# Kernel optimization log

Hardware: AMD Instinct MI355X
Metric: run time of the kernel (lower is better)

## Reference

```python
import jax, jax.numpy as jnp
import numpy as np

B, M, N, D = 32, 10, 1000, 128
DEMAND_SCALER, SPEED_SCALER, PREF_SCALER = 40.0, 1.0, 1.0


def _pos_encoding(m, d, dtype):
    # standard sinusoidal PE over agent positions 0..m-1
    pos = jnp.arange(m, dtype=dtype)[:, None]
    div = jnp.exp(jnp.arange(0, d, 2, dtype=dtype) * (-jnp.log(jnp.asarray(10000.0, dtype)) / d))
    ang = pos * div  # (m, d/2)
    return jnp.stack([jnp.sin(ang), jnp.cos(ang)], axis=-1).reshape(m, d)  # even=sin, odd=cos


def setup_inputs() -> dict:
    key = jax.random.key(0)
    ks = jax.random.split(key, 14)
    return {
        "locs": jax.random.uniform(ks[0], (B, M + N, 2), jnp.float32),
        "capacity": jax.random.uniform(ks[1], (B, M), jnp.float32),
        "speed": jax.random.uniform(ks[2], (B, M), jnp.float32),
        "demand": jax.random.uniform(ks[3], (B, 1, M + N), jnp.float32),
        "agents_preference": jax.random.uniform(ks[4], (B, M, M + N), jnp.float32),
        "action_mask": jnp.ones((B, M, M + N), dtype=bool),
        "W_depot": jax.random.normal(ks[5], (D, 2), jnp.float32) * 0.1,
        "W_posproj": jax.random.normal(ks[6], (D, D), jnp.float32) * 0.05,
        "alpha": jnp.ones((1,), jnp.float32),
        "W_agents": jax.random.normal(ks[7], (D, 4), jnp.float32) * 0.1,
        "W_depot_agents": jax.random.normal(ks[8], (D, 2 * D), jnp.float32) * 0.05,
        "W_clients": jax.random.normal(ks[9], (D, 5), jnp.float32) * 0.1,
        "W_pref": jax.random.normal(ks[10], (D, 1), jnp.float32) * 0.1,
        "W_final": jax.random.normal(ks[11], (D, 3 * D), jnp.float32) * 0.05,
    }


def reference(locs, capacity, speed, demand, agents_preference, action_mask,
              W_depot, W_posproj, alpha, W_agents, W_depot_agents, W_clients,
              W_pref, W_final):
    m = action_mask.shape[-2]
    d = W_final.shape[0]
    depot_locs = locs[:, :m]            # (B, m, 2)
    agents_locs = locs[:, :m]
    clients_locs = locs[:, m:]          # (B, N, 2)

    # depot branch with positional encoding
    dep_emb = depot_locs @ W_depot.T                                   # (B, m, D)
    pe = _pos_encoding(m, d, dep_emb.dtype)                            # (m, D)
    depot_embedding = dep_emb + alpha[0] * (pe @ W_posproj.T)          # broadcast over B

    # agents branch
    agents_feats = jnp.concatenate(
        [agents_locs, capacity[..., None] / DEMAND_SCALER, speed[..., None] / SPEED_SCALER], axis=-1)
    agents_embedding = agents_feats @ W_agents.T                       # (B, m, D)
    depot_agents_embedding = jnp.concatenate(
        [depot_embedding, agents_embedding], axis=-1) @ W_depot_agents.T  # (B, m, D)

    # clients branch (with polar feats)
    demands = demand[:, 0, m:]                                         # (B, N)
    centered = clients_locs - depot_locs[:, 0:1]                       # (B, N, 2)
    dist = jnp.linalg.norm(centered, axis=-1, keepdims=True)
    angle = jnp.arctan2(centered[..., 1:], centered[..., :1])
    clients_feats = jnp.concatenate(
        [clients_locs, demands[..., None] / DEMAND_SCALER, dist, angle], axis=-1)
    clients_embedding = clients_feats @ W_clients.T                    # (B, N, D)

    nodes_embedding = jnp.concatenate([agents_embedding, clients_embedding], axis=1)  # (B, m+N, D)

    # fused final projection: Linear(3D, D) on cat([nodes, pref_embed, depot_agents])
    # == nodes @ Wn.T  +  pref_embed @ Wp.T  +  depot_agents @ Wd.T, broadcast over dims.
    # pref_embed = pref[..., None] * W_pref[:, 0]  (rank-1), so pref_embed @ Wp.T = pref[..., None] * (Wp @ W_pref[:, 0])
    Wn, Wp, Wd = W_final[:, :d], W_final[:, d:2 * d], W_final[:, 2 * d:]
    v_pref = Wp @ W_pref[:, 0]                                         # (D,)
    pref = agents_preference / PREF_SCALER                             # (B, m, m+N)
    combined_embedding = (
        (nodes_embedding @ Wn.T)[:, None, :, :]                        # (B, 1, m+N, D)
        + pref[..., None] * v_pref                                     # (B, m, m+N, D)
        + (depot_agents_embedding @ Wd.T)[:, :, None, :]               # (B, m, 1, D)
    )
    return nodes_embedding, combined_embedding
```

## Files before the change

### kernel.cpp

```cpp
#include <hip/hip_runtime.h>
#include <math.h>

#define BB 32
#define MM 10
#define NNODES 1010
#define DD 128
#define RPB 32
#define NG 32

__global__ __launch_bounds__(256) void k_prep(
    const float* __restrict__ W_posproj,
    const float* __restrict__ W_da,
    const float* __restrict__ W_pref,
    const float* __restrict__ W_final,
    float* __restrict__ wnT,
    float* __restrict__ wdT,
    float* __restrict__ wdaT,
    float* __restrict__ vpref,
    float* __restrict__ peproj)
{
    const int bk = blockIdx.x;
    const int t = threadIdx.x;
    const int d = t & (DD - 1);
    const int h = t >> 7;

    if (bk < 16) {
        #pragma unroll
        for (int kk = 0; kk < 4; ++kk) {
            const int k = bk * 8 + h * 4 + kk;
            wnT[k * DD + d] = W_final[(size_t)d * 384 + k];
            wdT[k * DD + d] = W_final[(size_t)d * 384 + 256 + k];
        }
    } else if (bk < 32) {
        #pragma unroll
        for (int kk = 0; kk < 8; ++kk) {
            const int k = (bk - 16) * 16 + h * 8 + kk;
            wdaT[k * DD + d] = W_da[(size_t)d * 256 + k];
        }
    } else if (bk == 32) {
        if (t < DD) {
            float vp = 0.0f;
            const float4* w = (const float4*)(W_final + (size_t)d * 384 + DD);
            const float4* p = (const float4*)W_pref;
            #pragma unroll
            for (int k4 = 0; k4 < 32; ++k4) {
                const float4 a = w[k4], b = p[k4];
                vp = fmaf(a.x, b.x, fmaf(a.y, b.y, fmaf(a.z, b.z, fmaf(a.w, b.w, vp))));
            }
            vpref[d] = vp;
        }
    } else {
        const int m = bk - 33;
        __shared__ float pe_s[DD];
        if (t < DD) {
            const int i = d >> 1;
            const float div = expf((float)(2 * i) * (-logf(10000.0f) / (float)DD));
            const float ang = (float)m * div;
            pe_s[d] = (d & 1) ? cosf(ang) : sinf(ang);
        }
        __syncthreads();
        if (t < DD) {
            float pp = 0.0f;
            const float4* w = (const float4*)(W_posproj + (size_t)d * DD);
            const float4* p = (const float4*)pe_s;
            #pragma unroll
            for (int k4 = 0; k4 < 32; ++k4) {
                const float4 a = w[k4], b = p[k4];
                pp = fmaf(a.x, b.x, fmaf(a.y, b.y, fmaf(a.z, b.z, fmaf(a.w, b.w, pp))));
            }
            peproj[m * DD + d] = pp;
        }
    }
}

__global__ __launch_bounds__(256) void k_agents(
    const float* __restrict__ locs,
    const float* __restrict__ capacity,
    const float* __restrict__ speed,
    const float* __restrict__ W_depot,
    const float* __restrict__ alpha,
    const float* __restrict__ W_agents,
    const float* __restrict__ wdaT,
    const float* __restrict__ wdT,
    const float* __restrict__ peproj,
    float* __restrict__ out_nodes,
    float* __restrict__ ws_daWd)
{
    const int b = blockIdx.x / MM;
    const int m = blockIdx.x % MM;
    const int t = threadIdx.x;
    const int d = t & (DD - 1);
    const int h = t >> 7;

    __shared__ float cat_s[2 * DD];
    __shared__ float da_s[DD];
    __shared__ float part[2][DD];

    if (h == 0) {
        const float lx = locs[((size_t)b * NNODES + m) * 2 + 0];
        const float ly = locs[((size_t)b * NNODES + m) * 2 + 1];
        const float dep = fmaf(lx, W_depot[d * 2 + 0],
                          fmaf(ly, W_depot[d * 2 + 1],
                               alpha[0] * peproj[m * DD + d]));
        const float cap = capacity[b * MM + m] * (1.0f / 40.0f);
        const float spd = speed[b * MM + m];
        const float ag = fmaf(lx, W_agents[d * 4 + 0],
                         fmaf(ly, W_agents[d * 4 + 1],
                         fmaf(cap, W_agents[d * 4 + 2],
                              spd * W_agents[d * 4 + 3])));
        out_nodes[((size_t)b * NNODES + m) * DD + d] = ag;
        cat_s[d] = dep;
        cat_s[DD + d] = ag;
    }
    __syncthreads();

    {
        float a0 = 0.f, a1 = 0.f, a2 = 0.f, a3 = 0.f;
        const float* wp = wdaT + (size_t)(h * DD) * DD + d;
        const float* cp = cat_s + h * DD;
        #pragma unroll 8
        for (int k = 0; k < DD; k += 4) {
            a0 = fmaf(cp[k + 0], wp[(size_t)(k + 0) * DD], a0);
            a1 = fmaf(cp[k + 1], wp[(size_t)(k + 1) * DD], a1);
            a2 = fmaf(cp[k + 2], wp[(size_t)(k + 2) * DD], a2);
            a3 = fmaf(cp[k + 3], wp[(size_t)(k + 3) * DD], a3);
        }
        part[h][d] = (a0 + a1) + (a2 + a3);
    }
    __syncthreads();
    if (h == 0) da_s[d] = part[0][d] + part[1][d];
    __syncthreads();

    {
        float a0 = 0.f, a1 = 0.f, a2 = 0.f, a3 = 0.f;
        const float* wp = wdT + (size_t)(h * 64) * DD + d;
        const float* cp = da_s + h * 64;
        #pragma unroll 4
        for (int k = 0; k < 64; k += 4) {
            a0 = fmaf(cp[k + 0], wp[(size_t)(k + 0) * DD], a0);
            a1 = fmaf(cp[k + 1], wp[(size_t)(k + 1) * DD], a1);
            a2 = fmaf(cp[k + 2], wp[(size_t)(k + 2) * DD], a2);
            a3 = fmaf(cp[k + 3], wp[(size_t)(k + 3) * DD], a3);
        }
        part[h][d] = (a0 + a1) + (a2 + a3);
    }
    __syncthreads();
    if (h == 0)
        ws_daWd[(b * MM + m) * DD + d] = part[0][d] + part[1][d];
}

__global__ __launch_bounds__(256) void k_main(
    const float* __restrict__ locs,
    const float* __restrict__ demand,
    const float* __restrict__ pref,
    const float* __restrict__ W_clients,
    const float* __restrict__ wnT,
    const float* __restrict__ ws_daWd,
    const float* __restrict__ ws_vpref,
    float* __restrict__ out_nodes,
    float* __restrict__ out_comb)
{
    const int g = blockIdx.x;
    const int b = blockIdx.y;
    const int t = threadIdx.x;
    const int n0 = g * RPB;

    __shared__ float rows[RPB][DD];
    __shared__ float feat[RPB][5];
    __shared__ float pref_s[MM][RPB];

    if (t < RPB) {
        const int node = n0 + t;
        if (node < NNODES && node >= MM) {
            const float cx = locs[((size_t)b * NNODES + node) * 2 + 0];
            const float cy = locs[((size_t)b * NNODES + node) * 2 + 1];
            const float d0x = locs[((size_t)b * NNODES + 0) * 2 + 0];
            const float d0y = locs[((size_t)b * NNODES + 0) * 2 + 1];
            const float dx = cx - d0x;
            const float dy = cy - d0y;
            feat[t][0] = cx;
            feat[t][1] = cy;
            feat[t][2] = demand[(size_t)b * NNODES + node] * (1.0f / 40.0f);
            feat[t][3] = sqrtf(fmaf(dx, dx, dy * dy));
            feat[t][4] = atan2f(dy, dx);
        }
    }
    for (int idx = t; idx < MM * RPB; idx += 256) {
        const int mm = idx >> 5;
        const int rr = idx & 31;
        const int node = n0 + rr;
        pref_s[mm][rr] = (node < NNODES)
            ? pref[(size_t)(b * MM + mm) * NNODES + node] : 0.0f;
    }
    __syncthreads();

    {
        const int d = t & (DD - 1);
        const int h = t >> 7;
        const float wc0 = W_clients[d * 5 + 0];
        const float wc1 = W_clients[d * 5 + 1];
        const float wc2 = W_clients[d * 5 + 2];
        const float wc3 = W_clients[d * 5 + 3];
        const float wc4 = W_clients[d * 5 + 4];
        #pragma unroll
        for (int i = 0; i < RPB / 2; ++i) {
            const int r = h * (RPB / 2) + i;
            const int node = n0 + r;
            float val = 0.0f;
            if (node < NNODES) {
                if (node < MM) {
                    val = out_nodes[((size_t)b * NNODES + node) * DD + d];
                } else {
                    val = fmaf(feat[r][0], wc0,
                          fmaf(feat[r][1], wc1,
                          fmaf(feat[r][2], wc2,
                          fmaf(feat[r][3], wc3,
                               feat[r][4] * wc4))));
                    out_nodes[((size_t)b * NNODES + node) * DD + d] = val;
                }
            }
            rows[r][d] = val;
        }
    }
    __syncthreads();

    const int c = t & 31;
    const int s = t >> 5;
    const int col = c * 4;
    float4 acc[4];
    #pragma unroll
    for (int j = 0; j < 4; ++j) acc[j] = make_float4(0.f, 0.f, 0.f, 0.f);

    {
        const float* wt = wnT + col;
        #pragma unroll 2
        for (int k4 = 0; k4 < DD / 4; ++k4) {
            const float4 w0 = *(const float4*)(wt + (size_t)(k4 * 4 + 0) * DD);
            const float4 w1 = *(const float4*)(wt + (size_t)(k4 * 4 + 1) * DD);
            const float4 w2 = *(const float4*)(wt + (size_t)(k4 * 4 + 2) * DD);
            const float4 w3 = *(const float4*)(wt + (size_t)(k4 * 4 + 3) * DD);
            #pragma unroll
            for (int j = 0; j < 4; ++j) {
                const float4 x = *(const float4*)&rows[s * 4 + j][k4 * 4];
                acc[j].x = fmaf(x.x, w0.x, fmaf(x.y, w1.x,
                           fmaf(x.z, w2.x, fmaf(x.w, w3.x, acc[j].x))));
                acc[j].y = fmaf(x.x, w0.y, fmaf(x.y, w1.y,
                           fmaf(x.z, w2.y, fmaf(x.w, w3.y, acc[j].y))));
                acc[j].z = fmaf(x.x, w0.z, fmaf(x.y, w1.z,
                           fmaf(x.z, w2.z, fmaf(x.w, w3.z, acc[j].z))));
                acc[j].w = fmaf(x.x, w0.w, fmaf(x.y, w1.w,
                           fmaf(x.z, w2.w, fmaf(x.w, w3.w, acc[j].w))));
            }
        }
    }

    const float4 vp = *(const float4*)(ws_vpref + col);
    float4 dawd[MM];
    #pragma unroll
    for (int mm = 0; mm < MM; ++mm)
        dawd[mm] = *(const float4*)(ws_daWd + (size_t)(b * MM + mm) * DD + col);

    #pragma unroll
    for (int mm = 0; mm < MM; ++mm) {
        #pragma unroll
        for (int j = 0; j < 4; ++j) {
            const int node = n0 + s * 4 + j;
            if (node >= NNODES) continue;
            const float pr = pref_s[mm][s * 4 + j];
            float4 o;
            o.x = fmaf(pr, vp.x, acc[j].x + dawd[mm].x);
            o.y = fmaf(pr, vp.y, acc[j].y + dawd[mm].y);
            o.z = fmaf(pr, vp.z, acc[j].z + dawd[mm].z);
            o.w = fmaf(pr, vp.w, acc[j].w + dawd[mm].w);
            *(float4*)(out_comb +
                ((size_t)(b * MM + mm) * NNODES + node) * DD + col) = o;
        }
    }
}

extern "C" void kernel_launch(void* const* d_in, const int* in_sizes, int n_in,
                              void* d_out, int out_size, void* d_ws, size_t ws_size,
                              hipStream_t stream) {
    const float* locs        = (const float*)d_in[0];
    const float* capacity    = (const float*)d_in[1];
    const float* speed       = (const float*)d_in[2];
    const float* demand      = (const float*)d_in[3];
    const float* agents_pref = (const float*)d_in[4];
    const float* W_depot     = (const float*)d_in[6];
    const float* W_posproj   = (const float*)d_in[7];
    const float* alpha       = (const float*)d_in[8];
    const float* W_agents    = (const float*)d_in[9];
    const float* W_da        = (const float*)d_in[10];
    const float* W_clients   = (const float*)d_in[11];
    const float* W_pref      = (const float*)d_in[12];
    const float* W_final     = (const float*)d_in[13];

    float* out_nodes = (float*)d_out;
    float* out_comb  = out_nodes + (size_t)BB * NNODES * DD;

    float* ws_daWd  = (float*)d_ws;
    float* ws_vpref = ws_daWd + BB * MM * DD;
    float* ws_pepj  = ws_vpref + DD;
    float* ws_wnT   = ws_pepj + MM * DD;
    float* ws_wdT   = ws_wnT + DD * DD;
    float* ws_wdaT  = ws_wdT + DD * DD;

    k_prep<<<dim3(43), 256, 0, stream>>>(
        W_posproj, W_da, W_pref, W_final,
        ws_wnT, ws_wdT, ws_wdaT, ws_vpref, ws_pepj);

    k_agents<<<dim3(BB * MM), 256, 0, stream>>>(
        locs, capacity, speed, W_depot, alpha, W_agents,
        ws_wdaT, ws_wdT, ws_pepj, out_nodes, ws_daWd);

    k_main<<<dim3(NG, BB), 256, 0, stream>>>(
        locs, demand, agents_pref, W_clients, ws_wnT,
        ws_daWd, ws_vpref, out_nodes, out_comb);
}
```

Measured before the change: 234.3 us.

## Split main kernel into node-projection and broadcast-expand kernels with nontemporal stores

Splits the fused kernel in two. The first kernel computes node embeddings and the node-by-Wn projection and writes that projection to a padded workspace. The second kernel reads it back, adds the preference and depot-agent terms, and writes the large combined output with nontemporal stores so it does not pollute the cache. This adds a kernel launch and a workspace round-trip (about 16 MB) in exchange for a store-bound expand kernel free of GEMM register pressure.

```diff
diff --git a/kernel.cpp b/kernel.cpp
--- a/kernel.cpp
+++ b/kernel.cpp
@@ -7,6 +7,15 @@
 #define DD 128
 #define RPB 32
 #define NG 32
+#define NROWPAD 1024
+
+typedef float f4v __attribute__((ext_vector_type(4)));
+
+static __device__ __forceinline__ void nt_store4(float* p, float4 v) {
+    union { float4 a; f4v b; } u;
+    u.a = v;
+    __builtin_nontemporal_store(u.b, (f4v*)p);
+}
 
 __global__ __launch_bounds__(256) void k_prep(
     const float* __restrict__ W_posproj,
@@ -149,16 +158,13 @@
         ws_daWd[(b * MM + m) * DD + d] = part[0][d] + part[1][d];
 }
 
-__global__ __launch_bounds__(256) void k_main(
+__global__ __launch_bounds__(256) void k_nodes(
     const float* __restrict__ locs,
     const float* __restrict__ demand,
-    const float* __restrict__ pref,
     const float* __restrict__ W_clients,
     const float* __restrict__ wnT,
-    const float* __restrict__ ws_daWd,
-    const float* __restrict__ ws_vpref,
     float* __restrict__ out_nodes,
-    float* __restrict__ out_comb)
+    float* __restrict__ ws_nwn)
 {
     const int g = blockIdx.x;
     const int b = blockIdx.y;
@@ -167,7 +173,6 @@
 
     __shared__ float rows[RPB][DD];
     __shared__ float feat[RPB][5];
-    __shared__ float pref_s[MM][RPB];
 
     if (t < RPB) {
         const int node = n0 + t;
@@ -184,13 +189,6 @@
             feat[t][3] = sqrtf(fmaf(dx, dx, dy * dy));
             feat[t][4] = atan2f(dy, dx);
         }
-    }
-    for (int idx = t; idx < MM * RPB; idx += 256) {
-        const int mm = idx >> 5;
-        const int rr = idx & 31;
-        const int node = n0 + rr;
-        pref_s[mm][rr] = (node < NNODES)
-            ? pref[(size_t)(b * MM + mm) * NNODES + node] : 0.0f;
     }
     __syncthreads();
 
@@ -216,7 +214,8 @@
                           fmaf(feat[r][2], wc2,
                           fmaf(feat[r][3], wc3,
                                feat[r][4] * wc4))));
-                    out_nodes[((size_t)b * NNODES + node) * DD + d] = val;
+                    __builtin_nontemporal_store(val,
+                        out_nodes + ((size_t)b * NNODES + node) * DD + d);
                 }
             }
             rows[r][d] = val;
@@ -254,6 +253,46 @@
         }
     }
 
+    #pragma unroll
+    for (int j = 0; j < 4; ++j) {
+        const int node = n0 + s * 4 + j;
+        if (node < NNODES)
+            *(float4*)(ws_nwn + ((size_t)b * NROWPAD + node) * DD + col) = acc[j];
+    }
+}
+
+__global__ __launch_bounds__(256) void k_expand(
+    const float* __restrict__ pref,
+    const float* __restrict__ ws_nwn,
+    const float* __restrict__ ws_daWd,
+    const float* __restrict__ ws_vpref,
+    float* __restrict__ out_comb)
+{
+    const int g = blockIdx.x;
+    const int b = blockIdx.y;
+    const int t = threadIdx.x;
+    const int n0 = g * RPB;
+
+    __shared__ float pref_s[MM][RPB];
+    for (int idx = t; idx < MM * RPB; idx += 256) {
+        const int mm = idx >> 5;
+        const int rr = idx & 31;
+        const int node = n0 + rr;
+        pref_s[mm][rr] = (node < NNODES)
+            ? pref[(size_t)(b * MM + mm) * NNODES + node] : 0.0f;
+    }
+    __syncthreads();
+
+    const int c = t & 31;
+    const int s = t >> 5;
+    const int col = c * 4;
+
+    float4 nw[4];
+    #pragma unroll
+    for (int j = 0; j < 4; ++j)
+        nw[j] = *(const float4*)(ws_nwn +
+                    ((size_t)b * NROWPAD + n0 + s * 4 + j) * DD + col);
+
     const float4 vp = *(const float4*)(ws_vpref + col);
     float4 dawd[MM];
     #pragma unroll
@@ -268,12 +307,12 @@
             if (node >= NNODES) continue;
             const float pr = pref_s[mm][s * 4 + j];
             float4 o;
-            o.x = fmaf(pr, vp.x, acc[j].x + dawd[mm].x);
-            o.y = fmaf(pr, vp.y, acc[j].y + dawd[mm].y);
-            o.z = fmaf(pr, vp.z, acc[j].z + dawd[mm].z);
-            o.w = fmaf(pr, vp.w, acc[j].w + dawd[mm].w);
-            *(float4*)(out_comb +
-                ((size_t)(b * MM + mm) * NNODES + node) * DD + col) = o;
+            o.x = fmaf(pr, vp.x, nw[j].x + dawd[mm].x);
+            o.y = fmaf(pr, vp.y, nw[j].y + dawd[mm].y);
+            o.z = fmaf(pr, vp.z, nw[j].z + dawd[mm].z);
+            o.w = fmaf(pr, vp.w, nw[j].w + dawd[mm].w);
+            nt_store4(out_comb +
+                ((size_t)(b * MM + mm) * NNODES + node) * DD + col, o);
         }
     }
 }
@@ -304,6 +343,7 @@
     float* ws_wnT   = ws_pepj + MM * DD;
     float* ws_wdT   = ws_wnT + DD * DD;
     float* ws_wdaT  = ws_wdT + DD * DD;
+    float* ws_nwn   = ws_wdaT + 2 * DD * DD;
 
     k_prep<<<dim3(43), 256, 0, stream>>>(
         W_posproj, W_da, W_pref, W_final,
@@ -313,7 +353,9 @@
         locs, capacity, speed, W_depot, alpha, W_agents,
         ws_wdaT, ws_wdT, ws_pepj, out_nodes, ws_daWd);
 
-    k_main<<<dim3(NG, BB), 256, 0, stream>>>(
-        locs, demand, agents_pref, W_clients, ws_wnT,
-        ws_daWd, ws_vpref, out_nodes, out_comb);
-}
+    k_nodes<<<dim3(NG, BB), 256, 0, stream>>>(
+        locs, demand, W_clients, ws_wnT, out_nodes, ws_nwn);
+
+    k_expand<<<dim3(NG, BB), 256, 0, stream>>>(
+        agents_pref, ws_nwn, ws_daWd, ws_vpref, out_comb);
+}
```

Measured after the change: 255.7 us. +9.1%, slower.
